# Performance work log

Hardware: AMD Instinct MI355X
Metric: run time of the kernel (lower is better)

## Reference

```python
import jax, jax.numpy as jnp
import numpy as np
import math

B, N, D = 512, 256, 512

def setup_inputs() -> dict:
    key = jax.random.key(0)
    k0, k1, k2, k3 = jax.random.split(key, 4)
    scale = math.sqrt(6.0 / (D + D))  # xavier_uniform-like magnitude
    return {
        "msg_stacked": jax.random.normal(k0, (B, N, D), dtype=jnp.float32),
        "w_query": jax.random.uniform(k1, (D, D), dtype=jnp.float32, minval=-scale, maxval=scale),
        "w_key": jax.random.uniform(k2, (D, D), dtype=jnp.float32, minval=-scale, maxval=scale),
        "w_value": jax.random.uniform(k3, (D, D), dtype=jnp.float32, minval=-scale, maxval=scale),
    }

def reference(msg_stacked, w_query, w_key, w_value):
    norm = 1.0 / math.sqrt(w_key.shape[-1])
    q = jnp.einsum('bnd,de->bne', msg_stacked, w_query)
    k = jnp.einsum('bnd,de->bne', msg_stacked, w_key)
    v = jnp.einsum('bnd,de->bne', msg_stacked, w_value)
    scores = jnp.einsum('bne,bme->bnm', q, k) * norm
    attn = jax.nn.softmax(scores, axis=-1)
    # (attn @ v).sum(dim=1): sum over query positions n -> [B, D]
    merged = jnp.einsum('bnm,bme->be', attn, v)
    return merged
```

## Files before the change

kernel.cpp:

```cpp
#include <hip/hip_runtime.h>
#include <stdint.h>


typedef __attribute__((ext_vector_type(8))) short short8;
typedef __attribute__((ext_vector_type(4))) float f32x4;

#define MFMA16(a,b,c) __builtin_amdgcn_mfma_f32_16x16x32_bf16((a),(b),(c),0,0,0)

__device__ __forceinline__ uint16_t f2bf(float f){
  uint32_t x = __float_as_uint(f);
  uint32_t r = (x + 0x7FFFu + ((x >> 16) & 1u)) >> 16;
  return (uint16_t)r;
}

__global__ __launch_bounds__(256) void prep_a(const float* __restrict__ wq,
                                              const float* __restrict__ wk,
                                              uint16_t* __restrict__ aswz){
  __shared__ float sQ[64][17];
  __shared__ float sK[64][17];
  const int tid = threadIdx.x;
  const int k0 = blockIdx.y * 64, c0 = blockIdx.x * 64;
  const int tx = tid & 15, ty = tid >> 4;
  const int lr = tid >> 2, lc = (tid & 3) * 4;
  float acc[4][4] = {{0.f}};

  for (int e0 = 0; e0 < 512; e0 += 16){
    __syncthreads();
    float4 q4 = *(const float4*)(wq + (size_t)(k0 + lr) * 512 + e0 + lc);
    float4 k4 = *(const float4*)(wk + (size_t)(c0 + lr) * 512 + e0 + lc);
    sQ[lr][lc+0] = q4.x; sQ[lr][lc+1] = q4.y; sQ[lr][lc+2] = q4.z; sQ[lr][lc+3] = q4.w;
    sK[lr][lc+0] = k4.x; sK[lr][lc+1] = k4.y; sK[lr][lc+2] = k4.z; sK[lr][lc+3] = k4.w;
    __syncthreads();
    #pragma unroll
    for (int e = 0; e < 16; e++){
      float qv[4], kv[4];
      #pragma unroll
      for (int i = 0; i < 4; i++) qv[i] = sQ[ty + 16*i][e];
      #pragma unroll
      for (int j = 0; j < 4; j++) kv[j] = sK[tx + 16*j][e];
      #pragma unroll
      for (int i = 0; i < 4; i++)
        #pragma unroll
        for (int j = 0; j < 4; j++) acc[i][j] += qv[i] * kv[j];
    }
  }
  const float norm = 0.04419417382415922f;
  #pragma unroll
  for (int i = 0; i < 4; i++){
    #pragma unroll
    for (int j = 0; j < 4; j++){
      int k = k0 + ty + 16*i, c = c0 + tx + 16*j;
      int ks = k >> 5, q = (k >> 3) & 3, jj = k & 7, ct = c >> 4;
      int lane = q*16 + (c & 15);
      aswz[((size_t)((ct*16 + ks)*64 + lane))*8 + jj] = f2bf(acc[i][j] * norm);
    }
  }
}

__global__ __launch_bounds__(256,2) void gemm_T2(const float* __restrict__ msg,
                                                 const uint16_t* __restrict__ aswz,
                                                 uint16_t* __restrict__ T){
  __shared__ __align__(16) uint16_t sB[16384];
  __shared__ __align__(16) uint16_t sE[4][32][40];
  const int tid = threadIdx.x, w = tid >> 6, lane = tid & 63;
  const int l15 = lane & 15, q = lane >> 4;
  const int r0 = blockIdx.x * 128 + w * 32;

  short8 aLo[16], aHi[16];
  {
    const float* base0 = msg + (size_t)(r0 + l15) * 512 + q * 8;
    const float* base1 = msg + (size_t)(r0 + 16 + l15) * 512 + q * 8;
    #pragma unroll
    for (int ks = 0; ks < 16; ks++){
      float4 x0 = *(const float4*)(base0 + ks*32);
      float4 x1 = *(const float4*)(base0 + ks*32 + 4);
      float4 y0 = *(const float4*)(base1 + ks*32);
      float4 y1 = *(const float4*)(base1 + ks*32 + 4);
      short8 a, b;
      a[0]=(short)f2bf(x0.x); a[1]=(short)f2bf(x0.y); a[2]=(short)f2bf(x0.z); a[3]=(short)f2bf(x0.w);
      a[4]=(short)f2bf(x1.x); a[5]=(short)f2bf(x1.y); a[6]=(short)f2bf(x1.z); a[7]=(short)f2bf(x1.w);
      b[0]=(short)f2bf(y0.x); b[1]=(short)f2bf(y0.y); b[2]=(short)f2bf(y0.z); b[3]=(short)f2bf(y0.w);
      b[4]=(short)f2bf(y1.x); b[5]=(short)f2bf(y1.y); b[6]=(short)f2bf(y1.z); b[7]=(short)f2bf(y1.w);
      aLo[ks] = a; aHi[ks] = b;
    }
  }

  #pragma unroll 1
  for (int cg = 0; cg < 16; cg++){
    __syncthreads();
    {
      const uint4* gsrc = (const uint4*)(aswz + (size_t)cg * 16384);
      uint4* ldst = (uint4*)sB;
      #pragma unroll
      for (int p = 0; p < 8; p++)
        ldst[p*256 + tid] = gsrc[p*256 + tid];
    }
    __syncthreads();

    f32x4 a0 = {0.f,0.f,0.f,0.f}, a1 = {0.f,0.f,0.f,0.f};
    f32x4 a2 = {0.f,0.f,0.f,0.f}, a3 = {0.f,0.f,0.f,0.f};
    const uint16_t* b0p = sB + lane*8;
    const uint16_t* b1p = sB + 8192 + lane*8;
    #pragma unroll
    for (int ks = 0; ks < 16; ks++){
      short8 b0 = *(const short8*)(b0p + ks*512);
      short8 b1 = *(const short8*)(b1p + ks*512);
      a0 = MFMA16(aLo[ks], b0, a0);
      a1 = MFMA16(aLo[ks], b1, a1);
      a2 = MFMA16(aHi[ks], b0, a2);
      a3 = MFMA16(aHi[ks], b1, a3);
    }

    #pragma unroll
    for (int r = 0; r < 4; r++){
      sE[w][q*4 + r][l15]           = f2bf(a0[r]);
      sE[w][q*4 + r][16 + l15]      = f2bf(a1[r]);
      sE[w][16 + q*4 + r][l15]      = f2bf(a2[r]);
      sE[w][16 + q*4 + r][16 + l15] = f2bf(a3[r]);
    }
    #pragma unroll
    for (int pass = 0; pass < 2; pass++){
      int r2 = pass*16 + (lane >> 2);
      uint4 vv = *(const uint4*)&sE[w][r2][(lane & 3) * 8];
      *(uint4*)(T + (size_t)(r0 + r2) * 512 + cg*32 + (lane & 3) * 8) = vv;
    }
  }
}

__global__ __launch_bounds__(512) void attn_w(const uint16_t* __restrict__ T,
                                              const float* __restrict__ msg,
                                              float* __restrict__ w4){
  __shared__ uint16_t sP[64*520];
  __shared__ float sW[8][256];
  const int tid = threadIdx.x, w = tid >> 6, lane = tid & 63;
  const int l15 = lane & 15, q = lane >> 4;
  const int b = blockIdx.x >> 1, nh = blockIdx.x & 1;
  const int n0 = nh*128 + w*16;

  const uint16_t* abase = T + ((size_t)b*256 + n0 + l15) * 512 + q*8;
  short8 aT[16];
  #pragma unroll
  for (int ks = 0; ks < 16; ks++) aT[ks] = *(const short8*)(abase + ks*32);

  f32x4 acc[16];
  #pragma unroll
  for (int t = 0; t < 16; t++) acc[t] = (f32x4){0.f,0.f,0.f,0.f};

  for (int mp = 0; mp < 4; mp++){
    __syncthreads();
    #pragma unroll
    for (int it = 0; it < 16; it++){
      int idx = it*512 + tid;
      int row = idx >> 7, c4 = idx & 127;
      const float4 v = *(const float4*)(msg + ((size_t)b*256 + mp*64 + row)*512 + c4*4);
      uint2 pk;
      pk.x = (uint32_t)f2bf(v.x) | ((uint32_t)f2bf(v.y) << 16);
      pk.y = (uint32_t)f2bf(v.z) | ((uint32_t)f2bf(v.w) << 16);
      *(uint2*)(sP + row*520 + c4*4) = pk;
    }
    __syncthreads();
    #pragma unroll
    for (int ks = 0; ks < 16; ks++){
      const uint16_t* bp = sP + l15*520 + q*8 + ks*32;
      short8 b0 = *(const short8*)(bp);
      short8 b1 = *(const short8*)(bp + 16*520);
      short8 b2 = *(const short8*)(bp + 32*520);
      short8 b3 = *(const short8*)(bp + 48*520);
      acc[mp*4+0] = MFMA16(aT[ks], b0, acc[mp*4+0]);
      acc[mp*4+1] = MFMA16(aT[ks], b1, acc[mp*4+1]);
      acc[mp*4+2] = MFMA16(aT[ks], b2, acc[mp*4+2]);
      acc[mp*4+3] = MFMA16(aT[ks], b3, acc[mp*4+3]);
    }
  }

  float mx[4], inv[4];
  #pragma unroll
  for (int r = 0; r < 4; r++){
    float m_ = acc[0][r];
    #pragma unroll
    for (int t = 1; t < 16; t++) m_ = fmaxf(m_, acc[t][r]);
    m_ = fmaxf(m_, __shfl_xor(m_, 1));
    m_ = fmaxf(m_, __shfl_xor(m_, 2));
    m_ = fmaxf(m_, __shfl_xor(m_, 4));
    m_ = fmaxf(m_, __shfl_xor(m_, 8));
    mx[r] = m_;
  }
  #pragma unroll
  for (int t = 0; t < 16; t++){
    #pragma unroll
    for (int r = 0; r < 4; r++) acc[t][r] = __expf(acc[t][r] - mx[r]);
  }
  #pragma unroll
  for (int r = 0; r < 4; r++){
    float s_ = 0.f;
    #pragma unroll
    for (int t = 0; t < 16; t++) s_ += acc[t][r];
    s_ += __shfl_xor(s_, 1);
    s_ += __shfl_xor(s_, 2);
    s_ += __shfl_xor(s_, 4);
    s_ += __shfl_xor(s_, 8);
    inv[r] = 1.f / s_;
  }
  #pragma unroll
  for (int t = 0; t < 16; t++){
    float wc = acc[t][0]*inv[0] + acc[t][1]*inv[1] + acc[t][2]*inv[2] + acc[t][3]*inv[3];
    wc += __shfl_xor(wc, 16);
    wc += __shfl_xor(wc, 32);
    if (lane < 16) sW[w][t*16 + lane] = wc;
  }
  __syncthreads();
  if (tid < 256){
    float s = 0.f;
    #pragma unroll
    for (int ww = 0; ww < 8; ww++) s += sW[ww][tid];
    w4[(size_t)b*512 + nh*256 + tid] = s;
  }
}

__global__ __launch_bounds__(256) void final_merge(const float* __restrict__ msg,
                                                   const float* __restrict__ w4,
                                                   const float* __restrict__ wvm,
                                                   float* __restrict__ out){
  __shared__ float sWm[256];
  __shared__ float sU[512];
  const int tid = threadIdx.x, b = blockIdx.x;
  sWm[tid] = w4[(size_t)b*512 + tid] + w4[(size_t)b*512 + 256 + tid];
  __syncthreads();
  const float* mb = msg + (size_t)b * 131072;
  const int e0 = tid * 2;
  float u0 = 0.f, u1 = 0.f;
  #pragma unroll 4
  for (int m = 0; m < 256; m++){
    float wm = sWm[m];
    float2 m2 = *(const float2*)(mb + (size_t)m*512 + e0);
    u0 += wm * m2.x;
    u1 += wm * m2.y;
  }
  sU[e0] = u0; sU[e0+1] = u1;
  __syncthreads();
  float o0 = 0.f, o1 = 0.f;
  #pragma unroll 4
  for (int d = 0; d < 512; d++){
    float ud = sU[d];
    float2 wv2 = *(const float2*)(wvm + (size_t)d*512 + e0);
    o0 += ud * wv2.x; o1 += ud * wv2.y;
  }
  out[(size_t)b*512 + e0]     = o0;
  out[(size_t)b*512 + e0 + 1] = o1;
}

__device__ __forceinline__ void stage64(const float* __restrict__ src, uint16_t* dst, int tid){
  #pragma unroll 4
  for (int it = 0; it < 32; it++){
    int idx = it*256 + tid;
    int row = idx >> 7;
    int c4  = idx & 127;
    const float4 v = *(const float4*)(src + row*512 + c4*4);
    uint2 pk;
    pk.x = (uint32_t)f2bf(v.x) | ((uint32_t)f2bf(v.y) << 16);
    pk.y = (uint32_t)f2bf(v.z) | ((uint32_t)f2bf(v.w) << 16);
    *(uint2*)(dst + row*520 + c4*4) = pk;
  }
}

__global__ __launch_bounds__(256,1) void fused_attn(const float* __restrict__ msg,
                                                    const uint16_t* __restrict__ aswz,
                                                    const float* __restrict__ wvm,
                                                    float* __restrict__ out)
{
  __shared__ uint16_t sT[64*520];
  __shared__ uint16_t sStage[64*520];
  __shared__ float sW4[4][256];

  const int tid  = threadIdx.x;
  const int b    = blockIdx.x;
  const int lane = tid & 63;
  const int w    = tid >> 6;
  const int l15  = lane & 15;
  const int q    = lane >> 4;
  const float* mbp = msg + (size_t)b * (256*512);
  const short8* Ag = (const short8*)aswz;

  ((float*)sW4)[tid]       = 0.f;
  ((float*)sW4)[tid + 256] = 0.f;
  ((float*)sW4)[tid + 512] = 0.f;
  ((float*)sW4)[tid + 768] = 0.f;

  #pragma unroll 1
  for (int nc = 0; nc < 4; nc++){
    __syncthreads();
    stage64(mbp + nc*64*512, sStage, tid);
    __syncthreads();

    short8 aF[16];
    {
      const uint16_t* abase = sStage + (w*16 + l15)*520 + q*8;
      #pragma unroll
      for (int ks = 0; ks < 16; ks++) aF[ks] = *(const short8*)(abase + ks*32);
    }
    uint16_t* trow = sT + (w*16 + q*4)*520 + l15;
    for (int ct = 0; ct < 32; ct += 2){
      f32x4 a0 = {0.f,0.f,0.f,0.f}, a1 = {0.f,0.f,0.f,0.f};
      #pragma unroll
      for (int ks = 0; ks < 16; ks++){
        short8 b0 = Ag[(ct*16      + ks)*64 + lane];
        short8 b1 = Ag[(ct*16 + 16 + ks)*64 + lane];
        a0 = MFMA16(aF[ks], b0, a0);
        a1 = MFMA16(aF[ks], b1, a1);
      }
      #pragma unroll
      for (int r = 0; r < 4; r++){
        trow[r*520 + ct*16]      = f2bf(a0[r]);
        trow[r*520 + ct*16 + 16] = f2bf(a1[r]);
      }
    }

    f32x4 accS[16];
    #pragma unroll
    for (int t = 0; t < 16; t++) accS[t] = (f32x4){0.f,0.f,0.f,0.f};
    short8 aT[16];
    {
      const uint16_t* tbase = sT + (w*16 + l15)*520 + q*8;
      #pragma unroll
      for (int ks = 0; ks < 16; ks++) aT[ks] = *(const short8*)(tbase + ks*32);
    }
    #pragma unroll
    for (int mp = 0; mp < 4; mp++){
      __syncthreads();
      stage64(mbp + mp*64*512, sStage, tid);
      __syncthreads();
      const uint16_t* b0p = sStage + (     l15)*520 + q*8;
      const uint16_t* b1p = sStage + (16 + l15)*520 + q*8;
      const uint16_t* b2p = sStage + (32 + l15)*520 + q*8;
      const uint16_t* b3p = sStage + (48 + l15)*520 + q*8;
      #pragma unroll
      for (int ks = 0; ks < 16; ks++){
        short8 bb0 = *(const short8*)(b0p + ks*32);
        short8 bb1 = *(const short8*)(b1p + ks*32);
        short8 bb2 = *(const short8*)(b2p + ks*32);
        short8 bb3 = *(const short8*)(b3p + ks*32);
        accS[mp*4+0] = MFMA16(aT[ks], bb0, accS[mp*4+0]);
        accS[mp*4+1] = MFMA16(aT[ks], bb1, accS[mp*4+1]);
        accS[mp*4+2] = MFMA16(aT[ks], bb2, accS[mp*4+2]);
        accS[mp*4+3] = MFMA16(aT[ks], bb3, accS[mp*4+3]);
      }
    }

    float mx[4], inv[4];
    #pragma unroll
    for (int r = 0; r < 4; r++){
      float m_ = accS[0][r];
      #pragma unroll
      for (int t = 1; t < 16; t++) m_ = fmaxf(m_, accS[t][r]);
      m_ = fmaxf(m_, __shfl_xor(m_, 1));
      m_ = fmaxf(m_, __shfl_xor(m_, 2));
      m_ = fmaxf(m_, __shfl_xor(m_, 4));
      m_ = fmaxf(m_, __shfl_xor(m_, 8));
      mx[r] = m_;
    }
    #pragma unroll
    for (int t = 0; t < 16; t++){
      #pragma unroll
      for (int r = 0; r < 4; r++) accS[t][r] = __expf(accS[t][r] - mx[r]);
    }
    #pragma unroll
    for (int r = 0; r < 4; r++){
      float s_ = 0.f;
      #pragma unroll
      for (int t = 0; t < 16; t++) s_ += accS[t][r];
      s_ += __shfl_xor(s_, 1);
      s_ += __shfl_xor(s_, 2);
      s_ += __shfl_xor(s_, 4);
      s_ += __shfl_xor(s_, 8);
      inv[r] = 1.f / s_;
    }
    #pragma unroll
    for (int t = 0; t < 16; t++){
      float wc = accS[t][0]*inv[0] + accS[t][1]*inv[1] + accS[t][2]*inv[2] + accS[t][3]*inv[3];
      wc += __shfl_xor(wc, 16);
      wc += __shfl_xor(wc, 32);
      if (lane < 16) sW4[w][t*16 + lane] += wc;
    }
  }

  __syncthreads();
  {
    float wt = sW4[0][tid] + sW4[1][tid] + sW4[2][tid] + sW4[3][tid];
    sW4[0][tid] = wt;
  }
  __syncthreads();
  float u0 = 0.f, u1 = 0.f;
  for (int m = 0; m < 256; m++){
    float ww = sW4[0][m];
    u0 += ww * mbp[m*512 + tid];
    u1 += ww * mbp[m*512 + tid + 256];
  }
  float* sU = (float*)sStage;
  sU[tid] = u0; sU[tid + 256] = u1;
  __syncthreads();
  float o0 = 0.f, o1 = 0.f;
  for (int d = 0; d < 512; d++){
    float ud = sU[d];
    o0 += ud * wvm[(size_t)d*512 + tid];
    o1 += ud * wvm[(size_t)d*512 + tid + 256];
  }
  out[(size_t)b*512 + tid]       = o0;
  out[(size_t)b*512 + tid + 256] = o1;
}

extern "C" void kernel_launch(void* const* d_in, const int* in_sizes, int n_in,
                              void* d_out, int out_size, void* d_ws, size_t ws_size,
                              hipStream_t stream) {
  const float* msg = (const float*)d_in[0];
  const float* wq  = (const float*)d_in[1];
  const float* wk  = (const float*)d_in[2];
  const float* wv  = (const float*)d_in[3];

  const size_t SZ_A = 524288;
  const size_t SZ_T = 134217728;
  const size_t SZ_W = 1048576;
  const size_t REQ  = SZ_A + SZ_T + SZ_W;

  uint16_t* aswz = (uint16_t*)d_ws;
  prep_a<<<dim3(8,8), 256, 0, stream>>>(wq, wk, aswz);

  if (ws_size >= REQ){
    uint16_t* T  = (uint16_t*)((char*)d_ws + SZ_A);
    float*    w4 = (float*)   ((char*)d_ws + SZ_A + SZ_T);
    gemm_T2    <<<1024, 256, 0, stream>>>(msg, aswz, T);
    attn_w     <<<1024, 512, 0, stream>>>(T, msg, w4);
    final_merge<<<512, 256, 0, stream>>>(msg, w4, wv, (float*)d_out);
  } else {
    fused_attn<<<512, 256, 0, stream>>>(msg, aswz, wv, (float*)d_out);
  }
}
```

Measured before the change: 703.3 us.

## Pre-cast msg to bf16 MFMA-fragment layout once and reuse across kernels

Adds a cast kernel that converts msg to bf16 in the MFMA operand-fragment order, so the T GEMM, the attention-weight kernel and the final merge all read half-size pre-swizzled data instead of re-reading fp32 msg and converting it each time. T is also written in fragment layout, which lets the attention kernel load its operands with plain contiguous vector loads and stage LDS with straight copies. The cost is an extra launch, a 128MB extra workspace requirement (the fallback fused path runs if the workspace is too small), and a more complex split reduction in final_merge.

```diff
diff --git a/kernel.cpp b/kernel.cpp
--- a/kernel.cpp
+++ b/kernel.cpp
@@ -7,11 +7,11 @@
 
 #define MFMA16(a,b,c) __builtin_amdgcn_mfma_f32_16x16x32_bf16((a),(b),(c),0,0,0)
 
-__device__ __forceinline__ uint16_t f2bf(float f){
+__device__ __forceinline__ uint32_t f2bf(float f){
   uint32_t x = __float_as_uint(f);
-  uint32_t r = (x + 0x7FFFu + ((x >> 16) & 1u)) >> 16;
-  return (uint16_t)r;
-}
+  return (x + 0x7FFFu + ((x >> 16) & 1u)) >> 16;
+}
+__device__ __forceinline__ float bf2f(uint32_t h){ return __uint_as_float(h << 16); }
 
 __global__ __launch_bounds__(256) void prep_a(const float* __restrict__ wq,
                                               const float* __restrict__ wk,
@@ -52,37 +52,47 @@
       int k = k0 + ty + 16*i, c = c0 + tx + 16*j;
       int ks = k >> 5, q = (k >> 3) & 3, jj = k & 7, ct = c >> 4;
       int lane = q*16 + (c & 15);
-      aswz[((size_t)((ct*16 + ks)*64 + lane))*8 + jj] = f2bf(acc[i][j] * norm);
-    }
-  }
-}
-
-__global__ __launch_bounds__(256,2) void gemm_T2(const float* __restrict__ msg,
+      aswz[((size_t)((ct*16 + ks)*64 + lane))*8 + jj] = (uint16_t)f2bf(acc[i][j] * norm);
+    }
+  }
+}
+
+__global__ __launch_bounds__(256) void cast_msg_frag(const float* __restrict__ msg,
+                                                     uint16_t* __restrict__ mf){
+  const int tid = threadIdx.x, w = tid >> 6, lane = tid & 63;
+  const int l15 = lane & 15, q = lane >> 4;
+  const int rt = blockIdx.x * 4 + w;
+  const float* rowp = msg + (size_t)(rt*16 + l15) * 512;
+  uint16_t* dst = mf + (size_t)rt * 8192 + lane * 8;
+  #pragma unroll
+  for (int ks = 0; ks < 16; ks++){
+    const int col0 = ks*32 + q*8;
+    float4 a = *(const float4*)(rowp + col0);
+    float4 b = *(const float4*)(rowp + col0 + 4);
+    uint4 pk;
+    pk.x = f2bf(a.x) | (f2bf(a.y) << 16);
+    pk.y = f2bf(a.z) | (f2bf(a.w) << 16);
+    pk.z = f2bf(b.x) | (f2bf(b.y) << 16);
+    pk.w = f2bf(b.z) | (f2bf(b.w) << 16);
+    *(uint4*)(dst + ks*512) = pk;
+  }
+}
+
+__global__ __launch_bounds__(256,2) void gemm_T3(const uint16_t* __restrict__ mf,
                                                  const uint16_t* __restrict__ aswz,
-                                                 uint16_t* __restrict__ T){
+                                                 uint16_t* __restrict__ TF){
   __shared__ __align__(16) uint16_t sB[16384];
   __shared__ __align__(16) uint16_t sE[4][32][40];
   const int tid = threadIdx.x, w = tid >> 6, lane = tid & 63;
   const int l15 = lane & 15, q = lane >> 4;
-  const int r0 = blockIdx.x * 128 + w * 32;
+  const int rt0 = blockIdx.x * 8 + w * 2;
 
   short8 aLo[16], aHi[16];
   {
-    const float* base0 = msg + (size_t)(r0 + l15) * 512 + q * 8;
-    const float* base1 = msg + (size_t)(r0 + 16 + l15) * 512 + q * 8;
-    #pragma unroll
-    for (int ks = 0; ks < 16; ks++){
-      float4 x0 = *(const float4*)(base0 + ks*32);
-      float4 x1 = *(const float4*)(base0 + ks*32 + 4);
-      float4 y0 = *(const float4*)(base1 + ks*32);
-      float4 y1 = *(const float4*)(base1 + ks*32 + 4);
-      short8 a, b;
-      a[0]=(short)f2bf(x0.x); a[1]=(short)f2bf(x0.y); a[2]=(short)f2bf(x0.z); a[3]=(short)f2bf(x0.w);
-      a[4]=(short)f2bf(x1.x); a[5]=(short)f2bf(x1.y); a[6]=(short)f2bf(x1.z); a[7]=(short)f2bf(x1.w);
-      b[0]=(short)f2bf(y0.x); b[1]=(short)f2bf(y0.y); b[2]=(short)f2bf(y0.z); b[3]=(short)f2bf(y0.w);
-      b[4]=(short)f2bf(y1.x); b[5]=(short)f2bf(y1.y); b[6]=(short)f2bf(y1.z); b[7]=(short)f2bf(y1.w);
-      aLo[ks] = a; aHi[ks] = b;
-    }
+    const short8* A0 = (const short8*)(mf + (size_t)rt0 * 8192) + lane;
+    const short8* A1 = (const short8*)(mf + (size_t)(rt0+1) * 8192) + lane;
+    #pragma unroll
+    for (int ks = 0; ks < 16; ks++){ aLo[ks] = A0[ks*64]; aHi[ks] = A1[ks*64]; }
   }
 
   #pragma unroll 1
@@ -92,19 +102,16 @@
       const uint4* gsrc = (const uint4*)(aswz + (size_t)cg * 16384);
       uint4* ldst = (uint4*)sB;
       #pragma unroll
-      for (int p = 0; p < 8; p++)
-        ldst[p*256 + tid] = gsrc[p*256 + tid];
+      for (int p = 0; p < 8; p++) ldst[p*256 + tid] = gsrc[p*256 + tid];
     }
     __syncthreads();
 
     f32x4 a0 = {0.f,0.f,0.f,0.f}, a1 = {0.f,0.f,0.f,0.f};
     f32x4 a2 = {0.f,0.f,0.f,0.f}, a3 = {0.f,0.f,0.f,0.f};
-    const uint16_t* b0p = sB + lane*8;
-    const uint16_t* b1p = sB + 8192 + lane*8;
     #pragma unroll
     for (int ks = 0; ks < 16; ks++){
-      short8 b0 = *(const short8*)(b0p + ks*512);
-      short8 b1 = *(const short8*)(b1p + ks*512);
+      short8 b0 = *(const short8*)(sB + (ks*64 + lane)*8);
+      short8 b1 = *(const short8*)(sB + 8192 + (ks*64 + lane)*8);
       a0 = MFMA16(aLo[ks], b0, a0);
       a1 = MFMA16(aLo[ks], b1, a1);
       a2 = MFMA16(aHi[ks], b0, a2);
@@ -113,34 +120,34 @@
 
     #pragma unroll
     for (int r = 0; r < 4; r++){
-      sE[w][q*4 + r][l15]           = f2bf(a0[r]);
-      sE[w][q*4 + r][16 + l15]      = f2bf(a1[r]);
-      sE[w][16 + q*4 + r][l15]      = f2bf(a2[r]);
-      sE[w][16 + q*4 + r][16 + l15] = f2bf(a3[r]);
-    }
-    #pragma unroll
-    for (int pass = 0; pass < 2; pass++){
-      int r2 = pass*16 + (lane >> 2);
-      uint4 vv = *(const uint4*)&sE[w][r2][(lane & 3) * 8];
-      *(uint4*)(T + (size_t)(r0 + r2) * 512 + cg*32 + (lane & 3) * 8) = vv;
-    }
-  }
-}
-
-__global__ __launch_bounds__(512) void attn_w(const uint16_t* __restrict__ T,
-                                              const float* __restrict__ msg,
-                                              float* __restrict__ w4){
-  __shared__ uint16_t sP[64*520];
+      sE[w][q*4 + r][l15]           = (uint16_t)f2bf(a0[r]);
+      sE[w][q*4 + r][16 + l15]      = (uint16_t)f2bf(a1[r]);
+      sE[w][16 + q*4 + r][l15]      = (uint16_t)f2bf(a2[r]);
+      sE[w][16 + q*4 + r][16 + l15] = (uint16_t)f2bf(a3[r]);
+    }
+    uint4 v0 = *(const uint4*)&sE[w][l15][q*8];
+    uint4 v1 = *(const uint4*)&sE[w][16 + l15][q*8];
+    *(uint4*)(TF + (size_t)rt0 * 8192 + cg*512 + lane*8)     = v0;
+    *(uint4*)(TF + (size_t)(rt0+1) * 8192 + cg*512 + lane*8) = v1;
+  }
+}
+
+__global__ __launch_bounds__(512,2) void attn_w2(const uint16_t* __restrict__ TF,
+                                                 const uint16_t* __restrict__ mf,
+                                                 float* __restrict__ w4){
+  __shared__ __align__(16) uint16_t sP[32768];
   __shared__ float sW[8][256];
   const int tid = threadIdx.x, w = tid >> 6, lane = tid & 63;
   const int l15 = lane & 15, q = lane >> 4;
   const int b = blockIdx.x >> 1, nh = blockIdx.x & 1;
-  const int n0 = nh*128 + w*16;
-
-  const uint16_t* abase = T + ((size_t)b*256 + n0 + l15) * 512 + q*8;
+  const int rt_a = b*16 + nh*8 + w;
+
   short8 aT[16];
-  #pragma unroll
-  for (int ks = 0; ks < 16; ks++) aT[ks] = *(const short8*)(abase + ks*32);
+  {
+    const short8* A0 = (const short8*)(TF + (size_t)rt_a * 8192) + lane;
+    #pragma unroll
+    for (int ks = 0; ks < 16; ks++) aT[ks] = A0[ks*64];
+  }
 
   f32x4 acc[16];
   #pragma unroll
@@ -148,24 +155,19 @@
 
   for (int mp = 0; mp < 4; mp++){
     __syncthreads();
-    #pragma unroll
-    for (int it = 0; it < 16; it++){
-      int idx = it*512 + tid;
-      int row = idx >> 7, c4 = idx & 127;
-      const float4 v = *(const float4*)(msg + ((size_t)b*256 + mp*64 + row)*512 + c4*4);
-      uint2 pk;
-      pk.x = (uint32_t)f2bf(v.x) | ((uint32_t)f2bf(v.y) << 16);
-      pk.y = (uint32_t)f2bf(v.z) | ((uint32_t)f2bf(v.w) << 16);
-      *(uint2*)(sP + row*520 + c4*4) = pk;
+    {
+      const uint4* src = (const uint4*)(mf + ((size_t)b*16 + mp*4) * 8192);
+      uint4* dst = (uint4*)sP;
+      #pragma unroll
+      for (int it = 0; it < 8; it++) dst[it*512 + tid] = src[it*512 + tid];
     }
     __syncthreads();
     #pragma unroll
     for (int ks = 0; ks < 16; ks++){
-      const uint16_t* bp = sP + l15*520 + q*8 + ks*32;
-      short8 b0 = *(const short8*)(bp);
-      short8 b1 = *(const short8*)(bp + 16*520);
-      short8 b2 = *(const short8*)(bp + 32*520);
-      short8 b3 = *(const short8*)(bp + 48*520);
+      short8 b0 = *(const short8*)(sP + (      ks)*512 + lane*8);
+      short8 b1 = *(const short8*)(sP + (16 + ks)*512 + lane*8);
+      short8 b2 = *(const short8*)(sP + (32 + ks)*512 + lane*8);
+      short8 b3 = *(const short8*)(sP + (48 + ks)*512 + lane*8);
       acc[mp*4+0] = MFMA16(aT[ks], b0, acc[mp*4+0]);
       acc[mp*4+1] = MFMA16(aT[ks], b1, acc[mp*4+1]);
       acc[mp*4+2] = MFMA16(aT[ks], b2, acc[mp*4+2]);
@@ -217,27 +219,44 @@
   }
 }
 
-__global__ __launch_bounds__(256) void final_merge(const float* __restrict__ msg,
-                                                   const float* __restrict__ w4,
-                                                   const float* __restrict__ wvm,
-                                                   float* __restrict__ out){
+__global__ __launch_bounds__(256) void final_merge_f(const uint16_t* __restrict__ mf,
+                                                     const float* __restrict__ w4,
+                                                     const float* __restrict__ wvm,
+                                                     float* __restrict__ out){
   __shared__ float sWm[256];
+  __shared__ float sPart[16][516];
   __shared__ float sU[512];
   const int tid = threadIdx.x, b = blockIdx.x;
   sWm[tid] = w4[(size_t)b*512 + tid] + w4[(size_t)b*512 + 256 + tid];
   __syncthreads();
-  const float* mb = msg + (size_t)b * 131072;
+  const int l15 = tid & 15, g = tid >> 4;
+  const uint4* base = (const uint4*)(mf + (size_t)b * 16 * 8192);
+  #pragma unroll
+  for (int s = 0; s < 4; s++){
+    const int kq = g + 16*s;
+    const int ks = kq >> 2, qq = kq & 3;
+    float u8[8] = {0.f,0.f,0.f,0.f,0.f,0.f,0.f,0.f};
+    #pragma unroll 4
+    for (int mt = 0; mt < 16; mt++){
+      uint4 v = base[(mt*16 + ks)*64 + qq*16 + l15];
+      float wm = sWm[mt*16 + l15];
+      u8[0] += wm * bf2f(v.x & 0xFFFFu); u8[1] += wm * bf2f(v.x >> 16);
+      u8[2] += wm * bf2f(v.y & 0xFFFFu); u8[3] += wm * bf2f(v.y >> 16);
+      u8[4] += wm * bf2f(v.z & 0xFFFFu); u8[5] += wm * bf2f(v.z >> 16);
+      u8[6] += wm * bf2f(v.w & 0xFFFFu); u8[7] += wm * bf2f(v.w >> 16);
+    }
+    #pragma unroll
+    for (int j = 0; j < 8; j++) sPart[l15][kq*8 + j] = u8[j];
+  }
+  __syncthreads();
+  {
+    float u0 = 0.f, u1 = 0.f;
+    #pragma unroll
+    for (int l = 0; l < 16; l++){ u0 += sPart[l][2*tid]; u1 += sPart[l][2*tid+1]; }
+    sU[2*tid] = u0; sU[2*tid+1] = u1;
+  }
+  __syncthreads();
   const int e0 = tid * 2;
-  float u0 = 0.f, u1 = 0.f;
-  #pragma unroll 4
-  for (int m = 0; m < 256; m++){
-    float wm = sWm[m];
-    float2 m2 = *(const float2*)(mb + (size_t)m*512 + e0);
-    u0 += wm * m2.x;
-    u1 += wm * m2.y;
-  }
-  sU[e0] = u0; sU[e0+1] = u1;
-  __syncthreads();
   float o0 = 0.f, o1 = 0.f;
   #pragma unroll 4
   for (int d = 0; d < 512; d++){
@@ -257,8 +276,8 @@
     int c4  = idx & 127;
     const float4 v = *(const float4*)(src + row*512 + c4*4);
     uint2 pk;
-    pk.x = (uint32_t)f2bf(v.x) | ((uint32_t)f2bf(v.y) << 16);
-    pk.y = (uint32_t)f2bf(v.z) | ((uint32_t)f2bf(v.w) << 16);
+    pk.x = f2bf(v.x) | (f2bf(v.y) << 16);
+    pk.y = f2bf(v.z) | (f2bf(v.w) << 16);
     *(uint2*)(dst + row*520 + c4*4) = pk;
   }
 }
@@ -310,8 +329,8 @@
       }
       #pragma unroll
       for (int r = 0; r < 4; r++){
-        trow[r*520 + ct*16]      = f2bf(a0[r]);
-        trow[r*520 + ct*16 + 16] = f2bf(a1[r]);
+        trow[r*520 + ct*16]      = (uint16_t)f2bf(a0[r]);
+        trow[r*520 + ct*16 + 16] = (uint16_t)f2bf(a1[r]);
       }
     }
 
@@ -417,19 +436,22 @@
   const float* wv  = (const float*)d_in[3];
 
   const size_t SZ_A = 524288;
+  const size_t SZ_M = 134217728;
   const size_t SZ_T = 134217728;
   const size_t SZ_W = 1048576;
-  const size_t REQ  = SZ_A + SZ_T + SZ_W;
+  const size_t REQ  = SZ_A + SZ_M + SZ_T + SZ_W;
 
   uint16_t* aswz = (uint16_t*)d_ws;
   prep_a<<<dim3(8,8), 256, 0, stream>>>(wq, wk, aswz);
 
   if (ws_size >= REQ){
-    uint16_t* T  = (uint16_t*)((char*)d_ws + SZ_A);
-    float*    w4 = (float*)   ((char*)d_ws + SZ_A + SZ_T);
-    gemm_T2    <<<1024, 256, 0, stream>>>(msg, aswz, T);
-    attn_w     <<<1024, 512, 0, stream>>>(T, msg, w4);
-    final_merge<<<512, 256, 0, stream>>>(msg, w4, wv, (float*)d_out);
+    uint16_t* mf = (uint16_t*)((char*)d_ws + SZ_A);
+    uint16_t* TF = (uint16_t*)((char*)d_ws + SZ_A + SZ_M);
+    float*    w4 = (float*)   ((char*)d_ws + SZ_A + SZ_M + SZ_T);
+    cast_msg_frag<<<2048, 256, 0, stream>>>(msg, mf);
+    gemm_T3      <<<1024, 256, 0, stream>>>(mf, aswz, TF);
+    attn_w2      <<<1024, 512, 0, stream>>>(TF, mf, w4);
+    final_merge_f<<<512, 256, 0, stream>>>(mf, w4, wv, (float*)d_out);
   } else {
     fused_attn<<<512, 256, 0, stream>>>(msg, aswz, wv, (float*)d_out);
   }
```

Result: slower. 721.6 us (+2.6%).
